# Optimization experiments

Measured on AMD Instinct MI355X. Metric: run time of the kernel, lower is better.

Reference implementation:

```python
import jax, jax.numpy as jnp
import numpy as np

B, T, HID, MC, L, NCLS = 256, 128, 64, 30, 2, 100


def _flow(x, t, fW0, fb0, fW1, fb1, fW2, fb2, ftw):
    # Continuous affine coupling flow (stribor). x: [..., S, HID], t: [..., S, 1]
    hid = x.shape[-1]
    base = (jnp.arange(hid) < hid // 2).astype(x.dtype)  # ordered_0 mask
    for l in range(fW0.shape[0]):
        m = base if l % 2 == 0 else 1.0 - base
        z = x * m
        a = jnp.tanh(jnp.concatenate([z, t], -1) @ fW0[l] + fb0[l])
        a = jnp.tanh(a @ fW1[l] + fb1[l])
        ss = a @ fW2[l] + fb2[l]                      # [..., 2*hid]
        scale, shift = jnp.split(ss, 2, -1)
        t_scale, t_shift = jnp.split(jnp.tanh(t * ftw[l]), 2, -1)  # TimeTanh
        x = z + (1.0 - m) * (x * jnp.exp(scale * t_scale) + shift * t_shift)
    return x


def setup_inputs() -> dict:
    key = jax.random.key(0)
    ks = jax.random.split(key, 12)
    n = lambda k, s, sc=0.1: jax.random.normal(k, s, dtype=jnp.float32) * sc
    return {
        "times": jax.random.uniform(ks[0], (B, T, 1), dtype=jnp.float32),
        "marks": jax.random.randint(ks[1], (B, T, 1), 0, NCLS),
        "mask": jnp.ones((B, T, 1), jnp.float32),
        "u": jax.random.uniform(ks[2], (T, MC, 1), dtype=jnp.float32),
        "emb": n(ks[3], (NCLS, HID), 1.0),
        "fW0": n(ks[4], (L, HID + 1, HID)),
        "fb0": jnp.zeros((L, HID), jnp.float32),
        "fW1": n(ks[5], (L, HID, HID)),
        "fb1": jnp.zeros((L, HID), jnp.float32),
        "fW2": n(ks[6], (L, HID, 2 * HID)),
        "fb2": jnp.zeros((L, 2 * HID), jnp.float32),
        "ftw": n(ks[7], (L, 2 * HID), 1.0),
        "Wi": n(ks[8], (HID, 1)),
        "bi": jnp.zeros((1,), jnp.float32),
        "W_ih": n(ks[9], (4 * HID, 1 + HID)),
        "W_hh": n(ks[10], (4 * HID, HID)),
        "b_ih": jnp.zeros((4 * HID,), jnp.float32),
        "b_hh": jnp.zeros((4 * HID,), jnp.float32),
    }


def reference(times, marks, mask, u, emb, fW0, fb0, fW1, fb1, fW2, fb2, ftw,
              Wi, bi, W_ih, W_hh, b_ih, b_hh):
    Bn, Tn, _ = times.shape
    hid = emb.shape[1]
    mc = u.shape[1]
    marks_e = emb[marks[..., 0]]      # [B,T,hid]
    m1 = marks_e[:, 1]                # source uses marks[:, 1] every step (faithful)
    inten = lambda x: jax.nn.softplus(x @ Wi + bi)

    def step(carry, xs):
        h, c = carry                  # h,c: [B,hid]
        t, u_i = xs                   # t: [B,1], u_i: [mc,1]
        t3 = t[:, None, :]            # [B,1,1]
        ts = u_i[None] * t3           # [B,mc,1] MC time samples in [0,t)
        xb = jnp.broadcast_to(h[:, None, :], (Bn, mc, hid))
        path = _flow(xb, ts, fW0, fb0, fW1, fb1, fW2, fb2, ftw)   # [B,mc,hid]
        integral = inten(path).mean(1, keepdims=True) * t3        # [B,1,1]
        h2 = _flow(h[:, None, :], t3, fW0, fb0, fW1, fb1, fW2, fb2, ftw)  # [B,1,hid]
        lam = inten(h2)                                           # [B,1,1]
        gates = jnp.concatenate([t, m1], -1) @ W_ih.T + b_ih + h2[:, 0] @ W_hh.T + b_hh
        ig, fg, gg, og = jnp.split(gates, 4, -1)
        c_n = jax.nn.sigmoid(fg) * c + jax.nn.sigmoid(ig) * jnp.tanh(gg)
        h_n = jax.nn.sigmoid(og) * jnp.tanh(c_n)
        nll = -jnp.log(lam[:, 0]) + integral[:, 0]                # [B,1]
        return (h_n, c_n), (h2[:, 0], nll)

    h0 = jnp.zeros((Bn, hid), times.dtype)
    (_, _), (hidden, nll) = jax.lax.scan(step, (h0, h0), (jnp.swapaxes(times, 0, 1), u))
    hidden = jnp.swapaxes(hidden, 0, 1)                           # [B,T,hid]
    loss = (jnp.swapaxes(nll, 0, 1)[:, :, :] * mask[..., 0][..., None]).sum() / mask.sum()
    return loss, hidden
```

## Files before the change

### kernel.cpp

```cpp
#include <hip/hip_runtime.h>
#include <hip/hip_bf16.h>
#include <math.h>

#define Bn   256
#define Tn   128
#define HID  64
#define MCn  30

typedef __attribute__((ext_vector_type(8))) short bf16x8;
typedef __attribute__((ext_vector_type(4))) float f32x4;

__device__ __forceinline__ float rcp_(float x) { return __builtin_amdgcn_rcpf(x); }
__device__ __forceinline__ float tanhf_(float x) {
    float e = __expf(-2.0f * x);
    return __builtin_fmaf(2.0f, rcp_(1.0f + e), -1.0f);
}
__device__ __forceinline__ float sigmoidf_(float x) {
    return rcp_(1.0f + __expf(-x));
}
__device__ __forceinline__ float softplusf_(float z) {
    float e = __expf(-fabsf(z));
    return fmaxf(z, 0.0f) + __logf(1.0f + e);
}
__device__ __forceinline__ unsigned short f2b(float f) {
    union { float f; unsigned u; } v; v.f = f;
    unsigned r = v.u + 0x7FFF + ((v.u >> 16) & 1);
    return (unsigned short)(r >> 16);
}
__device__ __forceinline__ unsigned pk2(float a, float b) {
    union { __hip_bfloat162 h2; unsigned u; } cv;
    cv.h2 = __float22bfloat162_rn(make_float2(a, b));
    return cv.u;
}

extern "C" __global__ __launch_bounds__(256)
void prep_kernel(const int* __restrict__ marks, const float* __restrict__ mask,
                 const float* __restrict__ emb, const float* __restrict__ fW0,
                 const float* __restrict__ fW1, const float* __restrict__ fW2,
                 const float* __restrict__ fb0, const float* __restrict__ fb1,
                 const float* __restrict__ fb2, const float* __restrict__ ftw,
                 const float* __restrict__ Wi, const float* __restrict__ W_ih,
                 const float* __restrict__ W_hh,
                 const float* __restrict__ b_ih, const float* __restrict__ b_hh,
                 float* __restrict__ gc, float* __restrict__ invd,
                 float* __restrict__ parv, unsigned short* __restrict__ parwb,
                 float* __restrict__ seqw1T, float* __restrict__ seqw2T,
                 float* __restrict__ whh260)
{
    __shared__ float red[4];
    const int blk = blockIdx.x, tid = threadIdx.x;
    if (blk < Bn) {
        const int mark = marks[blk * Tn + 1];
        const float* er = emb + mark * HID;
        const float* wr = W_ih + tid * 65 + 1;
        float acc = b_ih[tid] + b_hh[tid];
        #pragma unroll
        for (int k = 0; k < HID; k++) acc += er[k] * wr[k];
        gc[blk * 256 + tid] = acc;
    } else if (blk == Bn) {
        float s = 0.f;
        for (int i = tid; i < Bn * Tn; i += 256) s += mask[i];
        #pragma unroll
        for (int off = 32; off >= 1; off >>= 1) s += __shfl_xor(s, off, 64);
        if ((tid & 63) == 0) red[tid >> 6] = s;
        __syncthreads();
        if (tid == 0) invd[0] = 1.0f / (red[0] + red[1] + red[2] + red[3]);
    } else if (blk == Bn + 1) {
        if (tid < 128) {
            int l = tid >> 6, m = tid & 63;
            parv[tid]       = fb0[tid];
            parv[128 + tid] = fW0[(l * 65 + 64) * 64 + m];
            parv[256 + tid] = fb1[tid];
            int act = 32 * (1 - l);
            parv[384 + tid] = fb2[l * 128 + act + (m & 31) + 64 * (m >> 5)];
        }
        if (tid < 64) {
            int l = tid >> 5, i2 = tid & 31, act = 32 * (1 - l);
            parv[512 + tid] = ftw[l * 128 + act + i2];
            parv[576 + tid] = ftw[l * 128 + 64 + act + i2];
            parv[640 + tid] = Wi[tid];
            parv[704 + tid] = 0.f;
        }
    } else if (blk == Bn + 2) {
        for (int i = tid; i < 5120; i += 256) {
            int k = i % 40, m = (i / 40) & 63, l = i / 2560;
            float v = (k < 32) ? fW0[(l * 65 + 32 * l + k) * 64 + m] : 0.f;
            parwb[i] = f2b(v);
        }
    } else if (blk == Bn + 3) {
        for (int i = tid; i < 9216; i += 256) {
            int k = i % 72, m = (i / 72) & 63, l = i / 4608;
            float v = (k < 64) ? fW1[(l * 64 + k) * 64 + m] : 0.f;
            parwb[5120 + i] = f2b(v);
        }
    } else if (blk == Bn + 4) {
        for (int i = tid; i < 9216; i += 256) {
            int k = i % 72, m = (i / 72) & 63, l = i / 4608;
            int act = 32 * (1 - l);
            float v = (k < 64) ? fW2[(l * 64 + k) * 128 + act + (m & 31) + 64 * (m >> 5)] : 0.f;
            parwb[14336 + i] = f2b(v);
        }
    } else if (blk == Bn + 5) {
        for (int i = tid; i < 8704; i += 256) {
            int k = i % 68, j = (i / 68) & 63, l = i / 4352;
            seqw1T[i] = (k < 64) ? fW1[(l * 64 + k) * 64 + j] : 0.f;
        }
    } else if (blk == Bn + 6) {
        for (int i = tid; i < 8704; i += 256) {
            int k = i % 68, j = (i / 68) & 63, l = i / 4352;
            int act = 32 * (1 - l);
            seqw2T[i] = (k < 64) ?
                fW2[(l * 64 + k) * 128 + act + (j & 31) + 64 * (j >> 5)] : 0.f;
        }
    } else {
        for (int i = tid; i < 16640; i += 256) {
            int j = i / 260, rem = i % 260, k = rem >> 2, r = rem & 3;
            whh260[i] = (k < 64) ? W_hh[(r * 64 + j) * 64 + k] : 0.f;
        }
    }
}

extern "C" __global__ __launch_bounds__(192, 1)
void fused_kernel(const float* __restrict__ times, const float* __restrict__ mask,
                  const float* __restrict__ u,
                  const float* __restrict__ fW0, const float* __restrict__ fb0,
                  const float* __restrict__ fb1, const float* __restrict__ fb2,
                  const float* __restrict__ ftw, const float* __restrict__ Wi,
                  const float* __restrict__ bi, const float* __restrict__ W_ih,
                  const float* __restrict__ gc, const float* __restrict__ seqw1T,
                  const float* __restrict__ parv,
                  const unsigned short* __restrict__ parwb,
                  const float* __restrict__ invd, float* __restrict__ out)
{
    const int tid  = threadIdx.x;
    const int lane = tid & 63;
    const int w    = tid >> 6;
    const int b    = blockIdx.x;
    const int quad = lane >> 4, l15 = lane & 15;

    extern __shared__ float smem[];
    float* w1l   = smem;
    float* w2l   = smem + 8704;
    float* whhl  = smem + 17408;
    float* tl    = smem + 34048;
    float* ml    = smem + 34176;
    float* xl    = smem + 34304;
    float* al    = smem + 34368;
    float* ssl   = smem + 34432;
    float* hbuf  = smem + 34496;
    float* h2buf = smem + 34624;
    float* pr    = smem + 34752;
    unsigned short* csact = (unsigned short*)(smem + 34756);
    unsigned short* csxk1 = csact + 2304;
    unsigned short* csx0  = csxk1 + 1280;

    {
        const float4* s = (const float4*)seqw1T;
        float4* d = (float4*)smem;
        for (int i = tid; i < 8512; i += 192) d[i] = s[i];
        for (int i = tid; i < 128; i += 192) {
            tl[i] = times[b * Tn + i];
            ml[i] = mask[b * Tn + i];
        }
    }

    const float bi0 = bi[0];
    const float idn = invd[0];
    const float wic = Wi[lane];

    float w0c[2][32], w0tc[2], b0c[2], b1c[2], b2c[2], ftsc[2], ftsh[2];
    float wih0[4], gcr[4];
    float h = 0.f, c_ = 0.f;
    if (w == 0) {
        #pragma unroll
        for (int l = 0; l < 2; l++) {
            #pragma unroll
            for (int kk = 0; kk < 32; kk++)
                w0c[l][kk] = fW0[(l * 65 + 32 * l + kk) * 64 + lane];
            w0tc[l] = fW0[(l * 65 + 64) * 64 + lane];
            b0c[l]  = fb0[l * 64 + lane];
            b1c[l]  = fb1[l * 64 + lane];
            const int act = 32 * (1 - l);
            b2c[l]  = fb2[l * 128 + act + (lane & 31) + 64 * (lane >> 5)];
            ftsc[l] = ftw[l * 128 + lane];
            ftsh[l] = ftw[l * 128 + 64 + lane];
        }
        #pragma unroll
        for (int r = 0; r < 4; r++) {
            wih0[r] = W_ih[(r * 64 + lane) * 65];
            gcr[r]  = gc[b * 256 + r * 64 + lane];
        }
    }
    const int cw = w - 1;
    unsigned short* myact = csact + cw * 1152;
    unsigned short* myxk  = csxk1 + cw * 640;
    unsigned short* myx0  = csx0  + cw * 40;
    const int mc  = cw * 16 + l15;
    const bool valmc = (w > 0) && (mc < MCn);
    float wacc = 0.f;
    float nllc = 0.f;

    __syncthreads();

    for (int t = 0; t < Tn; t++) {
        if (w == 0) hbuf[(t & 1) * 64 + lane] = h;
        __syncthreads();

        if (w == 0) {
            const float tb = tl[t];
            float tscv[2], tshv[2];
            #pragma unroll
            for (int l = 0; l < 2; l++) {
                tscv[l] = tanhf_(tb * ftsc[l]);
                tshv[l] = tanhf_(tb * ftsh[l]);
            }
            float x = h;
            xl[lane] = x;
            #pragma unroll
            for (int l = 0; l < 2; l++) {
                const int kb  = 32 * l;
                const int act = 32 * (1 - l);
                {
                    float p0 = b0c[l] + tb * w0tc[l], p1 = 0.f, p2 = 0.f, p3 = 0.f;
                    const float4* xv4 = (const float4*)(xl + kb);
                    #pragma unroll
                    for (int k4 = 0; k4 < 8; k4++) {
                        float4 xv = xv4[k4];
                        p0 += xv.x * w0c[l][4 * k4 + 0];
                        p1 += xv.y * w0c[l][4 * k4 + 1];
                        p2 += xv.z * w0c[l][4 * k4 + 2];
                        p3 += xv.w * w0c[l][4 * k4 + 3];
                    }
                    al[lane] = tanhf_((p0 + p1) + (p2 + p3));
                }
                {
                    float p0 = b1c[l], p1 = 0.f, p2 = 0.f, p3 = 0.f;
                    const float4* av4 = (const float4*)al;
                    const float*  wp  = w1l + (l * 64 + lane) * 68;
                    #pragma unroll
                    for (int k4 = 0; k4 < 16; k4++) {
                        float4 av = av4[k4];
                        float4 wv = *(const float4*)(wp + 4 * k4);
                        p0 += av.x * wv.x; p1 += av.y * wv.y;
                        p2 += av.z * wv.z; p3 += av.w * wv.w;
                    }
                    al[lane] = tanhf_((p0 + p1) + (p2 + p3));
                }
                {
                    float p0 = b2c[l], p1 = 0.f, p2 = 0.f, p3 = 0.f;
                    const float4* av4 = (const float4*)al;
                    const float*  wp  = w2l + (l * 64 + lane) * 68;
                    #pragma unroll
                    for (int k4 = 0; k4 < 16; k4++) {
                        float4 av = av4[k4];
                        float4 wv = *(const float4*)(wp + 4 * k4);
                        p0 += av.x * wv.x; p1 += av.y * wv.y;
                        p2 += av.z * wv.z; p3 += av.w * wv.w;
                    }
                    ssl[lane] = (p0 + p1) + (p2 + p3);
                }
                const int idx = (lane - act) & 31;
                const float scl = ssl[idx];
                const float shf = ssl[idx + 32];
                const float xa  = x * __expf(scl * tscv[l]) + shf * tshv[l];
                const bool active = (l == 0) ? (lane >= 32) : (lane < 32);
                x = active ? xa : x;
                xl[lane] = x;
            }
            h2buf[(t & 1) * 64 + lane] = x;
            const float tb2 = tb;
            float g0 = gcr[0] + tb2 * wih0[0];
            float g1 = gcr[1] + tb2 * wih0[1];
            float g2 = gcr[2] + tb2 * wih0[2];
            float g3 = gcr[3] + tb2 * wih0[3];
            {
                const float*  wr_base = whhl + lane * 260;
                const float4* hv4 = (const float4*)xl;
                #pragma unroll
                for (int k4 = 0; k4 < 16; k4++) {
                    float4 hv = hv4[k4];
                    const float* wr = wr_base + 16 * k4;
                    float4 wa = *(const float4*)(wr);
                    float4 wb = *(const float4*)(wr + 4);
                    float4 wc = *(const float4*)(wr + 8);
                    float4 wd = *(const float4*)(wr + 12);
                    g0 += hv.x * wa.x; g1 += hv.x * wa.y; g2 += hv.x * wa.z; g3 += hv.x * wa.w;
                    g0 += hv.y * wb.x; g1 += hv.y * wb.y; g2 += hv.y * wb.z; g3 += hv.y * wb.w;
                    g0 += hv.z * wc.x; g1 += hv.z * wc.y; g2 += hv.z * wc.z; g3 += hv.z * wc.w;
                    g0 += hv.w * wd.x; g1 += hv.w * wd.y; g2 += hv.w * wd.z; g3 += hv.w * wd.w;
                }
            }
            c_ = sigmoidf_(g1) * c_ + sigmoidf_(g0) * tanhf_(g2);
            h  = sigmoidf_(g3) * tanhf_(c_);
        } else {
            if (t > 0) {
                const int pt = t - 1;
                const float h2v = h2buf[(pt & 1) * 64 + lane];
                if (cw == 0) {
                    out[1 + (b * Tn + pt) * 64 + lane] = h2v;
                } else {
                    float v = h2v * wic;
                    #pragma unroll
                    for (int off = 32; off >= 1; off >>= 1) v += __shfl_xor(v, off, 64);
                    nllc += -__logf(softplusf_(v + bi0)) * ml[pt];
                }
            }
            const float tb = tl[t];
            const float ts   = valmc ? u[t * MCn + mc] * tb : 0.f;
            const float sclf = valmc ? tb * (1.0f / 30.0f) * idn * ml[t] : 0.f;
            const float* hb  = hbuf + (t & 1) * 64;
            f32x4 xr[4];
            #pragma unroll
            for (int mt = 0; mt < 4; mt++)
                xr[mt] = *(const f32x4*)(hb + mt * 16 + quad * 4);
            if (lane < 32) myx0[lane] = f2b(hb[lane]);
            #pragma unroll
            for (int l = 0; l < 2; l++) {
                const unsigned short* wA1 = parwb + l * 2560;
                const unsigned short* wA2 = parwb + 5120 + l * 4608;
                const unsigned short* wA3 = parwb + 14336 + l * 4608;
                f32x4 c1[4];
                {
                    bf16x8 bfin = (l == 0) ? *(const bf16x8*)(myx0 + quad * 8)
                                           : *(const bf16x8*)(myxk + l15 * 40 + quad * 8);
                    #pragma unroll
                    for (int mt = 0; mt < 4; mt++) {
                        bf16x8 af = *(const bf16x8*)(wA1 + (mt * 16 + l15) * 40 + quad * 8);
                        f32x4 z = {0.f, 0.f, 0.f, 0.f};
                        c1[mt] = __builtin_amdgcn_mfma_f32_16x16x32_bf16(af, bfin, z, 0, 0, 0);
                    }
                }
                #pragma unroll
                for (int mt = 0; mt < 4; mt++) {
                    f32x4 b0r = *(const f32x4*)(parv + 0   + l * 64 + mt * 16 + quad * 4);
                    f32x4 w0r = *(const f32x4*)(parv + 128 + l * 64 + mt * 16 + quad * 4);
                    float v0 = tanhf_(c1[mt][0] + b0r[0] + ts * w0r[0]);
                    float v1 = tanhf_(c1[mt][1] + b0r[1] + ts * w0r[1]);
                    float v2 = tanhf_(c1[mt][2] + b0r[2] + ts * w0r[2]);
                    float v3 = tanhf_(c1[mt][3] + b0r[3] + ts * w0r[3]);
                    uint2 pk; pk.x = pk2(v0, v1); pk.y = pk2(v2, v3);
                    *(uint2*)(myact + l15 * 72 + mt * 16 + quad * 4) = pk;
                }
                f32x4 cc[4];
                #pragma unroll
                for (int mt = 0; mt < 4; mt++) cc[mt] = (f32x4){0.f, 0.f, 0.f, 0.f};
                #pragma unroll
                for (int kt = 0; kt < 2; kt++) {
                    bf16x8 bfa = *(const bf16x8*)(myact + l15 * 72 + kt * 32 + quad * 8);
                    #pragma unroll
                    for (int mt = 0; mt < 4; mt++) {
                        bf16x8 af = *(const bf16x8*)(wA2 + (mt * 16 + l15) * 72 + kt * 32 + quad * 8);
                        cc[mt] = __builtin_amdgcn_mfma_f32_16x16x32_bf16(af, bfa, cc[mt], 0, 0, 0);
                    }
                }
                #pragma unroll
                for (int mt = 0; mt < 4; mt++) {
                    f32x4 b1r = *(const f32x4*)(parv + 256 + l * 64 + mt * 16 + quad * 4);
                    float v0 = tanhf_(cc[mt][0] + b1r[0]);
                    float v1 = tanhf_(cc[mt][1] + b1r[1]);
                    float v2 = tanhf_(cc[mt][2] + b1r[2]);
                    float v3 = tanhf_(cc[mt][3] + b1r[3]);
                    uint2 pk; pk.x = pk2(v0, v1); pk.y = pk2(v2, v3);
                    *(uint2*)(myact + l15 * 72 + mt * 16 + quad * 4) = pk;
                }
                f32x4 ssf[4];
                #pragma unroll
                for (int mt = 0; mt < 4; mt++) ssf[mt] = (f32x4){0.f, 0.f, 0.f, 0.f};
                #pragma unroll
                for (int kt = 0; kt < 2; kt++) {
                    bf16x8 bfa = *(const bf16x8*)(myact + l15 * 72 + kt * 32 + quad * 8);
                    #pragma unroll
                    for (int mt = 0; mt < 4; mt++) {
                        bf16x8 af = *(const bf16x8*)(wA3 + (mt * 16 + l15) * 72 + kt * 32 + quad * 8);
                        ssf[mt] = __builtin_amdgcn_mfma_f32_16x16x32_bf16(af, bfa, ssf[mt], 0, 0, 0);
                    }
                }
                #pragma unroll
                for (int mt2 = 0; mt2 < 2; mt2++) {
                    f32x4 b2s = *(const f32x4*)(parv + 384 + l * 64 +      mt2 * 16 + quad * 4);
                    f32x4 b2h = *(const f32x4*)(parv + 384 + l * 64 + 32 + mt2 * 16 + quad * 4);
                    f32x4 fa  = *(const f32x4*)(parv + 512 + l * 32 + mt2 * 16 + quad * 4);
                    f32x4 fb  = *(const f32x4*)(parv + 576 + l * 32 + mt2 * 16 + quad * 4);
                    const int xm = (l == 0) ? (mt2 + 2) : mt2;
                    #pragma unroll
                    for (int r = 0; r < 4; r++) {
                        float sc  = ssf[mt2][r] + b2s[r];
                        float sh  = ssf[mt2 + 2][r] + b2h[r];
                        float tsc = tanhf_(ts * fa[r]);
                        float tsh = tanhf_(ts * fb[r]);
                        xr[xm][r] = xr[xm][r] * __expf(sc * tsc) + sh * tsh;
                    }
                    if (l == 0) {
                        uint2 pk;
                        pk.x = pk2(xr[xm][0], xr[xm][1]);
                        pk.y = pk2(xr[xm][2], xr[xm][3]);
                        *(uint2*)(myxk + l15 * 40 + mt2 * 16 + quad * 4) = pk;
                    }
                }
            }
            float d0 = 0.f, d1 = 0.f;
            #pragma unroll
            for (int mt = 0; mt < 4; mt++) {
                f32x4 wi4 = *(const f32x4*)(parv + 640 + mt * 16 + quad * 4);
                d0 += xr[mt][0] * wi4[0] + xr[mt][2] * wi4[2];
                d1 += xr[mt][1] * wi4[1] + xr[mt][3] * wi4[3];
            }
            float d = d0 + d1;
            d += __shfl_xor(d, 16, 64);
            d += __shfl_xor(d, 32, 64);
            if (quad == 0) wacc += softplusf_(d + bi0) * sclf;
        }
    }

    __syncthreads();
    if (w > 0) {
        const int pt = Tn - 1;
        const float h2v = h2buf[(pt & 1) * 64 + lane];
        if (cw == 0) {
            out[1 + (b * Tn + pt) * 64 + lane] = h2v;
        } else {
            float v = h2v * wic;
            #pragma unroll
            for (int off = 32; off >= 1; off >>= 1) v += __shfl_xor(v, off, 64);
            nllc += -__logf(softplusf_(v + bi0)) * ml[pt];
        }
    }

    if (w == 0) {
        if (lane == 0) pr[0] = 0.f;
    } else {
        #pragma unroll
        for (int off = 1; off <= 32; off <<= 1) wacc += __shfl_xor(wacc, off, 64);
        if (lane == 0) pr[w] = wacc + ((cw == 1) ? nllc * idn : 0.f);
    }
    __syncthreads();
    if (tid == 0) atomicAdd(out, pr[0] + pr[1] + pr[2]);
}

extern "C" void kernel_launch(void* const* d_in, const int* in_sizes, int n_in,
                              void* d_out, int out_size, void* d_ws, size_t ws_size,
                              hipStream_t stream)
{
    const float* times = (const float*)d_in[0];
    const int*   marks = (const int*)  d_in[1];
    const float* mask  = (const float*)d_in[2];
    const float* u     = (const float*)d_in[3];
    const float* emb   = (const float*)d_in[4];
    const float* fW0   = (const float*)d_in[5];
    const float* fb0   = (const float*)d_in[6];
    const float* fW1   = (const float*)d_in[7];
    const float* fb1   = (const float*)d_in[8];
    const float* fW2   = (const float*)d_in[9];
    const float* fb2   = (const float*)d_in[10];
    const float* ftw   = (const float*)d_in[11];
    const float* Wi    = (const float*)d_in[12];
    const float* bi    = (const float*)d_in[13];
    const float* W_ih  = (const float*)d_in[14];
    const float* W_hh  = (const float*)d_in[15];
    const float* b_ih  = (const float*)d_in[16];
    const float* b_hh  = (const float*)d_in[17];
    float* out = (float*)d_out;

    float* wsp     = (float*)d_ws;
    float* gc      = wsp;
    float* invd    = gc + 65536;
    float* seqw1T  = invd + 4;
    float* seqw2T  = seqw1T + 8704;
    float* whh260  = seqw2T + 8704;
    float* parv    = whh260 + 16640;
    unsigned short* parwb = (unsigned short*)(parv + 768);

    hipMemsetAsync(d_out, 0, sizeof(float), stream);

    const int FUSED_SMEM = 34756 * 4 + 7328;
    hipFuncSetAttribute((const void*)fused_kernel,
                        hipFuncAttributeMaxDynamicSharedMemorySize, FUSED_SMEM);

    prep_kernel<<<Bn + 8, 256, 0, stream>>>(marks, mask, emb, fW0, fW1, fW2,
                                            fb0, fb1, fb2, ftw, Wi, W_ih, W_hh,
                                            b_ih, b_hh, gc, invd, parv, parwb,
                                            seqw1T, seqw2T, whh260);
    fused_kernel<<<Bn, 192, FUSED_SMEM, stream>>>(times, mask, u, fW0, fb0,
                                                  fb1, fb2, ftw, Wi, bi, W_ih,
                                                  gc, seqw1T, parv, parwb,
                                                  invd, out);
}
```

Before: 651.5 us.

## Replace per-step block barriers with LDS flag handshakes and a 4-slot ring

Each timestep no longer ends with a __syncthreads. Wave 0, which runs the serial flow and LSTM recurrence, now publishes h and h2 into 4-deep LDS ring buffers and bumps a volatile step counter. The two Monte Carlo waves spin on that counter with s_sleep and post their own progress flags. This lets the recurrence wave run up to a few steps ahead of the integral waves, so their work overlaps instead of meeting at a barrier every step. The cost is spin-polling overhead and the usual risks of hand-rolled LDS flag synchronization.

```diff
diff --git a/kernel.cpp b/kernel.cpp
--- a/kernel.cpp
+++ b/kernel.cpp
@@ -148,11 +148,10 @@
     float* al    = smem + 34368;
     float* ssl   = smem + 34432;
     float* hbuf  = smem + 34496;
-    float* h2buf = smem + 34624;
-    float* pr    = smem + 34752;
-    unsigned short* csact = (unsigned short*)(smem + 34756);
-    unsigned short* csxk1 = csact + 2304;
-    unsigned short* csx0  = csxk1 + 1280;
+    float* h2buf = smem + 34752;
+    float* pr    = smem + 35008;
+    volatile unsigned* flg = (volatile unsigned*)(smem + 35012);
+    unsigned short* cbase = (unsigned short*)(smem + 35016);
 
     {
         const float4* s = (const float4*)seqw1T;
@@ -162,6 +161,7 @@
             tl[i] = times[b * Tn + i];
             ml[i] = mask[b * Tn + i];
         }
+        if (tid < 3) flg[tid] = 0;
     }
 
     const float bi0 = bi[0];
@@ -192,9 +192,9 @@
         }
     }
     const int cw = w - 1;
-    unsigned short* myact = csact + cw * 1152;
-    unsigned short* myxk  = csxk1 + cw * 640;
-    unsigned short* myx0  = csx0  + cw * 40;
+    unsigned short* myact = cbase + cw * 1832;
+    unsigned short* myxk  = myact + 1152;
+    unsigned short* myx0  = myxk + 640;
     const int mc  = cw * 16 + l15;
     const bool valmc = (w > 0) && (mc < MCn);
     float wacc = 0.f;
@@ -202,11 +202,15 @@
 
     __syncthreads();
 
-    for (int t = 0; t < Tn; t++) {
-        if (w == 0) hbuf[(t & 1) * 64 + lane] = h;
-        __syncthreads();
-
-        if (w == 0) {
+    if (w == 0) {
+        for (int t = 0; t < Tn; t++) {
+            if (t >= 3) {
+                const unsigned need = (unsigned)(t - 2);
+                while (flg[1] < need || flg[2] < need) __builtin_amdgcn_s_sleep(1);
+                __threadfence_block();
+            }
+            hbuf[(t & 3) * 64 + lane] = h;
+            if (lane == 0) flg[0] = (unsigned)(t + 1);
             const float tb = tl[t];
             float tscv[2], tshv[2];
             #pragma unroll
@@ -267,12 +271,11 @@
                 x = active ? xa : x;
                 xl[lane] = x;
             }
-            h2buf[(t & 1) * 64 + lane] = x;
-            const float tb2 = tb;
-            float g0 = gcr[0] + tb2 * wih0[0];
-            float g1 = gcr[1] + tb2 * wih0[1];
-            float g2 = gcr[2] + tb2 * wih0[2];
-            float g3 = gcr[3] + tb2 * wih0[3];
+            h2buf[(t & 3) * 64 + lane] = x;
+            float g0 = gcr[0] + tb * wih0[0];
+            float g1 = gcr[1] + tb * wih0[1];
+            float g2 = gcr[2] + tb * wih0[2];
+            float g3 = gcr[3] + tb * wih0[3];
             {
                 const float*  wr_base = whhl + lane * 260;
                 const float4* hv4 = (const float4*)xl;
@@ -292,10 +295,15 @@
             }
             c_ = sigmoidf_(g1) * c_ + sigmoidf_(g0) * tanhf_(g2);
             h  = sigmoidf_(g3) * tanhf_(c_);
-        } else {
+        }
+        if (lane == 0) flg[0] = (unsigned)(Tn + 1);
+    } else {
+        for (int t = 0; t < Tn; t++) {
+            while (flg[0] < (unsigned)(t + 1)) __builtin_amdgcn_s_sleep(1);
+            __threadfence_block();
             if (t > 0) {
                 const int pt = t - 1;
-                const float h2v = h2buf[(pt & 1) * 64 + lane];
+                const float h2v = h2buf[(pt & 3) * 64 + lane];
                 if (cw == 0) {
                     out[1 + (b * Tn + pt) * 64 + lane] = h2v;
                 } else {
@@ -308,7 +316,7 @@
             const float tb = tl[t];
             const float ts   = valmc ? u[t * MCn + mc] * tb : 0.f;
             const float sclf = valmc ? tb * (1.0f / 30.0f) * idn * ml[t] : 0.f;
-            const float* hb  = hbuf + (t & 1) * 64;
+            const float* hb  = hbuf + (t & 3) * 64;
             f32x4 xr[4];
             #pragma unroll
             for (int mt = 0; mt < 4; mt++)
@@ -409,20 +417,21 @@
             d += __shfl_xor(d, 16, 64);
             d += __shfl_xor(d, 32, 64);
             if (quad == 0) wacc += softplusf_(d + bi0) * sclf;
-        }
-    }
-
-    __syncthreads();
-    if (w > 0) {
-        const int pt = Tn - 1;
-        const float h2v = h2buf[(pt & 1) * 64 + lane];
-        if (cw == 0) {
-            out[1 + (b * Tn + pt) * 64 + lane] = h2v;
-        } else {
-            float v = h2v * wic;
-            #pragma unroll
-            for (int off = 32; off >= 1; off >>= 1) v += __shfl_xor(v, off, 64);
-            nllc += -__logf(softplusf_(v + bi0)) * ml[pt];
+            if (lane == 0) flg[w] = (unsigned)(t + 1);
+        }
+        while (flg[0] < (unsigned)(Tn + 1)) __builtin_amdgcn_s_sleep(1);
+        __threadfence_block();
+        {
+            const int pt = Tn - 1;
+            const float h2v = h2buf[(pt & 3) * 64 + lane];
+            if (cw == 0) {
+                out[1 + (b * Tn + pt) * 64 + lane] = h2v;
+            } else {
+                float v = h2v * wic;
+                #pragma unroll
+                for (int off = 32; off >= 1; off >>= 1) v += __shfl_xor(v, off, 64);
+                nllc += -__logf(softplusf_(v + bi0)) * ml[pt];
+            }
         }
     }
 
@@ -472,7 +481,7 @@
 
     hipMemsetAsync(d_out, 0, sizeof(float), stream);
 
-    const int FUSED_SMEM = 34756 * 4 + 7328;
+    const int FUSED_SMEM = 35016 * 4 + 7328;
     hipFuncSetAttribute((const void*)fused_kernel,
                         hipFuncAttributeMaxDynamicSharedMemorySize, FUSED_SMEM);
 
```

Measured after the change: 612.2 us. 1.06x faster.
